# Optimization experiments

Measured on AMD Instinct MI355X. Metric: run time of the kernel, lower is better.

The kernel has to match this reference:

```python
import jax, jax.numpy as jnp
import numpy as np

T, DIM, E, INTER, TOPK = 4096, 1024, 8, 1408, 2


def setup_inputs() -> dict:
    key = jax.random.key(0)
    k_x, k_idx, k1, k2, k3 = jax.random.split(key, 5)
    scale = 1.0 / np.sqrt(DIM)
    return {
        "x": jax.random.normal(k_x, (T, DIM), dtype=jnp.float32),
        "expert_indices": jax.random.randint(k_idx, (T, TOPK), 0, E, dtype=jnp.int64),
        "w1": jax.random.normal(k1, (E, INTER, DIM), dtype=jnp.float32) * scale,
        "w2": jax.random.normal(k2, (E, DIM, INTER), dtype=jnp.float32) * scale,
        "w3": jax.random.normal(k3, (E, INTER, DIM), dtype=jnp.float32) * scale,
    }


def reference(x, expert_indices, w1, w2, w3):
    # All-expert SwiGLU FFN: [T, E, INTER]
    x1 = jax.nn.silu(jnp.einsum('ti,eoi->teo', x, w1))
    x3 = jnp.einsum('ti,eoi->teo', x, w3)
    # Down-projection per expert: [T, E, DIM]
    expert_outs = jnp.einsum('teo,eio->tei', x1 * x3, w2)
    # Gather only the routed experts per token: [T, TOPK, DIM]
    return jnp.take_along_axis(expert_outs, expert_indices[:, :, None], axis=1)
```

## Files before the change

### kernel.cpp

```cpp
#include <hip/hip_runtime.h>

#define TTOK   4096
#define DIMK   1024
#define NEXP   8
#define INTERN 1408
#define NPAIRS 8192

#define BM  128
#define BN  128
#define BK  64
#define NTH 256
#define NTG 512
#define MAXRT (NPAIRS / BM + NEXP - 1)
#define NT1  (INTERN / BN)
#define NT2  (DIMK / BN)

#define CVTBLKS 4096
#define N8X (TTOK * DIMK / 8)
#define N8W (NEXP * INTERN * DIMK / 8)

typedef __attribute__((ext_vector_type(8))) _Float16 half8;
typedef __attribute__((ext_vector_type(2))) _Float16 half2v;
typedef __attribute__((ext_vector_type(4))) float f32x4;

#define MFMAF16(a, b, c) __builtin_amdgcn_mfma_f32_16x16x32_f16((a), (b), (c), 0, 0, 0)

__device__ __forceinline__ void gl_lds16(const void* g, void* l) {
  __builtin_amdgcn_global_load_lds(
      (const __attribute__((address_space(1))) void*)g,
      (__attribute__((address_space(3))) void*)l, 16, 0, 0);
}

__device__ __forceinline__ int xcd_swz(int orig, int G) {
  int q = G >> 3, r = G & 7, x = orig & 7, p = orig >> 3;
  return (x < r ? x * (q + 1) : r * (q + 1) + (x - r) * q) + p;
}

__device__ __forceinline__ void cvt8(const float* __restrict__ src,
                                     unsigned short* __restrict__ dst,
                                     int n8, int tid, int stride) {
  const f32x4* s4 = reinterpret_cast<const f32x4*>(src);
  uint4* d4 = reinterpret_cast<uint4*>(dst);
  for (int i = tid; i < n8; i += stride) {
    f32x4 a = s4[2 * i], b = s4[2 * i + 1];
    uint4 o;
    o.x = __builtin_bit_cast(unsigned int, __builtin_amdgcn_cvt_pkrtz(a[0], a[1]));
    o.y = __builtin_bit_cast(unsigned int, __builtin_amdgcn_cvt_pkrtz(a[2], a[3]));
    o.z = __builtin_bit_cast(unsigned int, __builtin_amdgcn_cvt_pkrtz(b[0], b[1]));
    o.w = __builtin_bit_cast(unsigned int, __builtin_amdgcn_cvt_pkrtz(b[2], b[3]));
    d4[i] = o;
  }
}

__global__ __launch_bounds__(NTH) void prep_kernel(
    const float* __restrict__ x, const float* __restrict__ w1,
    const float* __restrict__ w3, const float* __restrict__ w2,
    unsigned short* __restrict__ xf, unsigned short* __restrict__ w1f,
    unsigned short* __restrict__ w3f, unsigned short* __restrict__ w2f,
    const int* __restrict__ ei, int* __restrict__ offs, int* __restrict__ pairs) {
  const int t = threadIdx.x;

  if (blockIdx.x == CVTBLKS) {
    __shared__ int cnt[NEXP], base[NEXP], cur[NEXP], mode;
    if (t == 0) mode = 0;
    if (t < NEXP) cnt[t] = 0;
    __syncthreads();
    int any = 0;
    for (int i = t; i < NPAIRS / 2; i += NTH) any |= ei[2 * i + 1];
    if (any) atomicOr(&mode, 1);
    __syncthreads();
    const int m32 = mode;
    for (int i = t; i < NPAIRS; i += NTH) {
      int e = (m32 ? ei[i] : ei[2 * i]) & (NEXP - 1);
      atomicAdd(&cnt[e], 1);
    }
    __syncthreads();
    if (t == 0) {
      int s = 0;
      for (int e = 0; e < NEXP; ++e) { base[e] = s; offs[e] = s; s += cnt[e]; }
      offs[NEXP] = s;
    }
    __syncthreads();
    if (t < NEXP) cur[t] = base[t];
    __syncthreads();
    for (int i = t; i < NPAIRS; i += NTH) {
      int e = (m32 ? ei[i] : ei[2 * i]) & (NEXP - 1);
      int p = atomicAdd(&cur[e], 1);
      pairs[p] = i;
    }
    return;
  }

  const int tid = blockIdx.x * NTH + t;
  const int stride = CVTBLKS * NTH;
  cvt8(x,  xf,  N8X, tid, stride);
  cvt8(w1, w1f, N8W, tid, stride);
  cvt8(w3, w3f, N8W, tid, stride);
  cvt8(w2, w2f, N8W, tid, stride);
}

__device__ __forceinline__ bool find_tile(const int* __restrict__ offs, int rt,
                                          int &e, int &row0, int &row_end) {
  int cum = 0;
  for (int i = 0; i < NEXP; ++i) {
    int b = offs[i], en = offs[i + 1];
    int nt = (en - b + BM - 1) / BM;
    if (rt < cum + nt) { e = i; row0 = b + (rt - cum) * BM; row_end = en; return true; }
    cum += nt;
  }
  return false;
}

__global__ __launch_bounds__(NTG, 4) void gemm1_kernel(
    const unsigned short* __restrict__ xf, const unsigned short* __restrict__ w1f,
    const unsigned short* __restrict__ w3f, const int* __restrict__ offs,
    const int* __restrict__ pairs, unsigned short* __restrict__ hf) {
  __shared__ __align__(16) unsigned short At[BM * BK];
  __shared__ __align__(16) unsigned short B1t[BN * BK];
  __shared__ __align__(16) unsigned short B3t[BN * BK];

  const int lid = xcd_swz((int)blockIdx.x, MAXRT * NT1);
  const int rt = lid % MAXRT, nt = lid / MAXRT;
  int e, row0, row_end;
  if (!find_tile(offs, rt, e, row0, row_end)) return;
  const int n0 = nt * BN;
  const int t = threadIdx.x;
  const int ln = t & 63;
  const int wv = t >> 6;
  const int wm = wv >> 2, wn = wv & 3;
  const int fr = ln & 15, fg = ln >> 4;
  const int sr = ln >> 3, sc = ln & 7;
  const int sw = (sc ^ sr) * 8;

  size_t aA[2], aB[2];
#pragma unroll
  for (int c = 0; c < 2; ++c) {
    int row = wv * 16 + c * 8 + sr;
    int p = row0 + row;
    int tok = ((p < row_end) ? pairs[p] : pairs[row0]) >> 1;
    aA[c] = (size_t)tok * DIMK + sw;
    aB[c] = ((size_t)e * INTERN + n0 + row) * DIMK + sw;
  }

  f32x4 acc1[4][2] = {};
  f32x4 acc3[4][2] = {};

  for (int k0 = 0; k0 < DIMK; k0 += BK) {
#pragma unroll
    for (int c = 0; c < 2; ++c)
      gl_lds16(xf + aA[c] + k0, &At[(wv * 16 + c * 8) * BK]);
#pragma unroll
    for (int c = 0; c < 2; ++c)
      gl_lds16(w1f + aB[c] + k0, &B1t[(wv * 16 + c * 8) * BK]);
#pragma unroll
    for (int c = 0; c < 2; ++c)
      gl_lds16(w3f + aB[c] + k0, &B3t[(wv * 16 + c * 8) * BK]);
    __syncthreads();

#pragma unroll
    for (int kk = 0; kk < 2; ++kk) {
      half8 ah[4];
#pragma unroll
      for (int m = 0; m < 4; ++m) {
        int row = wm * 64 + m * 16 + fr;
        ah[m] = *reinterpret_cast<const half8*>(
            &At[row * BK + (((kk * 4 + fg) ^ (fr & 7)) * 8)]);
      }
#pragma unroll
      for (int n = 0; n < 2; ++n) {
        int row = wn * 32 + n * 16 + fr;
        int bo = row * BK + (((kk * 4 + fg) ^ (fr & 7)) * 8);
        half8 b1 = *reinterpret_cast<const half8*>(&B1t[bo]);
        half8 b3 = *reinterpret_cast<const half8*>(&B3t[bo]);
#pragma unroll
        for (int m = 0; m < 4; ++m) {
          acc1[m][n] = MFMAF16(ah[m], b1, acc1[m][n]);
          acc3[m][n] = MFMAF16(ah[m], b3, acc3[m][n]);
        }
      }
    }
    __syncthreads();
  }

#pragma unroll
  for (int m = 0; m < 4; ++m)
#pragma unroll
    for (int n = 0; n < 2; ++n)
#pragma unroll
      for (int r = 0; r < 4; ++r) {
        int p = row0 + wm * 64 + m * 16 + fg * 4 + r;
        if (p < row_end) {
          int col = n0 + wn * 32 + n * 16 + fr;
          float a1 = acc1[m][n][r], a3 = acc3[m][n][r];
          float hv = (a1 / (1.0f + __expf(-a1))) * a3;
          hf[(size_t)p * INTERN + col] =
              __builtin_bit_cast(unsigned short, (_Float16)hv);
        }
      }
}

__global__ __launch_bounds__(NTG, 4) void gemm2_kernel(
    const unsigned short* __restrict__ w2f, const int* __restrict__ offs,
    const int* __restrict__ pairs, const unsigned short* __restrict__ hf,
    float* __restrict__ out) {
  __shared__ __align__(16) unsigned short At[BM * BK];
  __shared__ __align__(16) unsigned short Bt[BN * BK];

  const int lid = xcd_swz((int)blockIdx.x, MAXRT * NT2);
  const int rt = lid % MAXRT, nt = lid / MAXRT;
  int e, row0, row_end;
  if (!find_tile(offs, rt, e, row0, row_end)) return;
  const int n0 = nt * BN;
  const int t = threadIdx.x;
  const int ln = t & 63;
  const int wv = t >> 6;
  const int wm = wv >> 2, wn = wv & 3;
  const int fr = ln & 15, fg = ln >> 4;
  const int sr = ln >> 3, sc = ln & 7;
  const int sw = (sc ^ sr) * 8;

  size_t aA[2], aB[2];
#pragma unroll
  for (int c = 0; c < 2; ++c) {
    int row = wv * 16 + c * 8 + sr;
    int p = row0 + row;
    int ar = (p < row_end) ? p : row0;
    aA[c] = (size_t)ar * INTERN + sw;
    aB[c] = ((size_t)e * DIMK + n0 + row) * INTERN + sw;
  }

  f32x4 acc[4][2] = {};

  for (int k0 = 0; k0 < INTERN; k0 += BK) {
#pragma unroll
    for (int c = 0; c < 2; ++c)
      gl_lds16(hf + aA[c] + k0, &At[(wv * 16 + c * 8) * BK]);
#pragma unroll
    for (int c = 0; c < 2; ++c)
      gl_lds16(w2f + aB[c] + k0, &Bt[(wv * 16 + c * 8) * BK]);
    __syncthreads();

#pragma unroll
    for (int kk = 0; kk < 2; ++kk) {
      half8 ah[4];
#pragma unroll
      for (int m = 0; m < 4; ++m) {
        int row = wm * 64 + m * 16 + fr;
        ah[m] = *reinterpret_cast<const half8*>(
            &At[row * BK + (((kk * 4 + fg) ^ (fr & 7)) * 8)]);
      }
#pragma unroll
      for (int n = 0; n < 2; ++n) {
        int row = wn * 32 + n * 16 + fr;
        half8 b = *reinterpret_cast<const half8*>(
            &Bt[row * BK + (((kk * 4 + fg) ^ (fr & 7)) * 8)]);
#pragma unroll
        for (int m = 0; m < 4; ++m)
          acc[m][n] = MFMAF16(ah[m], b, acc[m][n]);
      }
    }
    __syncthreads();
  }

#pragma unroll
  for (int m = 0; m < 4; ++m)
#pragma unroll
    for (int n = 0; n < 2; ++n)
#pragma unroll
      for (int r = 0; r < 4; ++r) {
        int p = row0 + wm * 64 + m * 16 + fg * 4 + r;
        if (p < row_end) {
          int orow = pairs[p];
          out[(size_t)orow * DIMK + n0 + wn * 32 + n * 16 + fr] = acc[m][n][r];
        }
      }
}

extern "C" void kernel_launch(void* const* d_in, const int* in_sizes, int n_in,
                              void* d_out, int out_size, void* d_ws, size_t ws_size,
                              hipStream_t stream) {
  const float* x  = (const float*)d_in[0];
  const int*   ei = (const int*)d_in[1];
  const float* w1 = (const float*)d_in[2];
  const float* w2 = (const float*)d_in[3];
  const float* w3 = (const float*)d_in[4];
  float* out = (float*)d_out;

  char* ws = (char*)d_ws;
  int* offs  = (int*)ws;
  int* pairs = (int*)(ws + 256);

  const size_t sz_x = (size_t)TTOK * DIMK;
  const size_t sz_w = (size_t)NEXP * INTERN * DIMK;
  size_t off = 65536;
  unsigned short* x_f  = (unsigned short*)(ws + off); off += sz_x * 2;
  unsigned short* w1_f = (unsigned short*)(ws + off); off += sz_w * 2;
  unsigned short* w3_f = (unsigned short*)(ws + off); off += sz_w * 2;
  unsigned short* w2_f = (unsigned short*)(ws + off); off += sz_w * 2;
  unsigned short* h_f  = (unsigned short*)(ws + off);

  prep_kernel<<<CVTBLKS + 1, NTH, 0, stream>>>(
      x, w1, w3, w2, x_f, w1_f, w3_f, w2_f, ei, offs, pairs);
  gemm1_kernel<<<MAXRT * NT1, NTG, 0, stream>>>(x_f, w1_f, w3_f, offs, pairs, h_f);
  gemm2_kernel<<<MAXRT * NT2, NTG, 0, stream>>>(w2_f, offs, pairs, h_f, out);
}
```

Measured before the change: 301.4 us.

## Fuse fp32-to-fp16 weight conversion into GEMM tile loads instead of prepass

Drops the separate prepass that converted all three expert weight tensors to fp16 in global memory. Each GEMM now reads fp32 weights directly, converts them in registers and writes them swizzled into LDS, while x is still converted in a smaller prepass. This removes a full write and re-read of the fp16 weight copies. In exchange, weight tiles are read redundantly in fp32 by every row tile, and the synchronous register-staged loads replace the async global-to-LDS copies.

```diff
diff --git a/kernel.cpp b/kernel.cpp
--- a/kernel.cpp
+++ b/kernel.cpp
@@ -15,12 +15,10 @@
 #define NT1  (INTERN / BN)
 #define NT2  (DIMK / BN)
 
-#define CVTBLKS 4096
+#define XCVB 512
 #define N8X (TTOK * DIMK / 8)
-#define N8W (NEXP * INTERN * DIMK / 8)
 
 typedef __attribute__((ext_vector_type(8))) _Float16 half8;
-typedef __attribute__((ext_vector_type(2))) _Float16 half2v;
 typedef __attribute__((ext_vector_type(4))) float f32x4;
 
 #define MFMAF16(a, b, c) __builtin_amdgcn_mfma_f32_16x16x32_f16((a), (b), (c), 0, 0, 0)
@@ -36,12 +34,59 @@
   return (x < r ? x * (q + 1) : r * (q + 1) + (x - r) * q) + p;
 }
 
-__device__ __forceinline__ void cvt8(const float* __restrict__ src,
-                                     unsigned short* __restrict__ dst,
-                                     int n8, int tid, int stride) {
-  const f32x4* s4 = reinterpret_cast<const f32x4*>(src);
-  uint4* d4 = reinterpret_cast<uint4*>(dst);
-  for (int i = tid; i < n8; i += stride) {
+__device__ __forceinline__ void stage_cvt8(const float* __restrict__ src,
+                                           unsigned short* __restrict__ dst) {
+  f32x4 a = *reinterpret_cast<const f32x4*>(src);
+  f32x4 b = *reinterpret_cast<const f32x4*>(src + 4);
+  uint4 o;
+  o.x = __builtin_bit_cast(unsigned int, __builtin_amdgcn_cvt_pkrtz(a[0], a[1]));
+  o.y = __builtin_bit_cast(unsigned int, __builtin_amdgcn_cvt_pkrtz(a[2], a[3]));
+  o.z = __builtin_bit_cast(unsigned int, __builtin_amdgcn_cvt_pkrtz(b[0], b[1]));
+  o.w = __builtin_bit_cast(unsigned int, __builtin_amdgcn_cvt_pkrtz(b[2], b[3]));
+  *reinterpret_cast<uint4*>(dst) = o;
+}
+
+__global__ __launch_bounds__(NTH) void prep_kernel(
+    const float* __restrict__ x, unsigned short* __restrict__ xf,
+    const int* __restrict__ ei, int* __restrict__ offs, int* __restrict__ pairs) {
+  const int t = threadIdx.x;
+
+  if (blockIdx.x == XCVB) {
+    __shared__ int cnt[NEXP], base[NEXP], cur[NEXP], mode;
+    if (t == 0) mode = 0;
+    if (t < NEXP) cnt[t] = 0;
+    __syncthreads();
+    int any = 0;
+    for (int i = t; i < NPAIRS / 2; i += NTH) any |= ei[2 * i + 1];
+    if (any) atomicOr(&mode, 1);
+    __syncthreads();
+    const int m32 = mode;
+    for (int i = t; i < NPAIRS; i += NTH) {
+      int e = (m32 ? ei[i] : ei[2 * i]) & (NEXP - 1);
+      atomicAdd(&cnt[e], 1);
+    }
+    __syncthreads();
+    if (t == 0) {
+      int s = 0;
+      for (int e = 0; e < NEXP; ++e) { base[e] = s; offs[e] = s; s += cnt[e]; }
+      offs[NEXP] = s;
+    }
+    __syncthreads();
+    if (t < NEXP) cur[t] = base[t];
+    __syncthreads();
+    for (int i = t; i < NPAIRS; i += NTH) {
+      int e = (m32 ? ei[i] : ei[2 * i]) & (NEXP - 1);
+      int p = atomicAdd(&cur[e], 1);
+      pairs[p] = i;
+    }
+    return;
+  }
+
+  const int tid = blockIdx.x * NTH + t;
+  const int stride = XCVB * NTH;
+  const f32x4* s4 = reinterpret_cast<const f32x4*>(x);
+  uint4* d4 = reinterpret_cast<uint4*>(xf);
+  for (int i = tid; i < N8X; i += stride) {
     f32x4 a = s4[2 * i], b = s4[2 * i + 1];
     uint4 o;
     o.x = __builtin_bit_cast(unsigned int, __builtin_amdgcn_cvt_pkrtz(a[0], a[1]));
@@ -50,53 +95,6 @@
     o.w = __builtin_bit_cast(unsigned int, __builtin_amdgcn_cvt_pkrtz(b[2], b[3]));
     d4[i] = o;
   }
-}
-
-__global__ __launch_bounds__(NTH) void prep_kernel(
-    const float* __restrict__ x, const float* __restrict__ w1,
-    const float* __restrict__ w3, const float* __restrict__ w2,
-    unsigned short* __restrict__ xf, unsigned short* __restrict__ w1f,
-    unsigned short* __restrict__ w3f, unsigned short* __restrict__ w2f,
-    const int* __restrict__ ei, int* __restrict__ offs, int* __restrict__ pairs) {
-  const int t = threadIdx.x;
-
-  if (blockIdx.x == CVTBLKS) {
-    __shared__ int cnt[NEXP], base[NEXP], cur[NEXP], mode;
-    if (t == 0) mode = 0;
-    if (t < NEXP) cnt[t] = 0;
-    __syncthreads();
-    int any = 0;
-    for (int i = t; i < NPAIRS / 2; i += NTH) any |= ei[2 * i + 1];
-    if (any) atomicOr(&mode, 1);
-    __syncthreads();
-    const int m32 = mode;
-    for (int i = t; i < NPAIRS; i += NTH) {
-      int e = (m32 ? ei[i] : ei[2 * i]) & (NEXP - 1);
-      atomicAdd(&cnt[e], 1);
-    }
-    __syncthreads();
-    if (t == 0) {
-      int s = 0;
-      for (int e = 0; e < NEXP; ++e) { base[e] = s; offs[e] = s; s += cnt[e]; }
-      offs[NEXP] = s;
-    }
-    __syncthreads();
-    if (t < NEXP) cur[t] = base[t];
-    __syncthreads();
-    for (int i = t; i < NPAIRS; i += NTH) {
-      int e = (m32 ? ei[i] : ei[2 * i]) & (NEXP - 1);
-      int p = atomicAdd(&cur[e], 1);
-      pairs[p] = i;
-    }
-    return;
-  }
-
-  const int tid = blockIdx.x * NTH + t;
-  const int stride = CVTBLKS * NTH;
-  cvt8(x,  xf,  N8X, tid, stride);
-  cvt8(w1, w1f, N8W, tid, stride);
-  cvt8(w3, w3f, N8W, tid, stride);
-  cvt8(w2, w2f, N8W, tid, stride);
 }
 
 __device__ __forceinline__ bool find_tile(const int* __restrict__ offs, int rt,
@@ -112,8 +110,8 @@
 }
 
 __global__ __launch_bounds__(NTG, 4) void gemm1_kernel(
-    const unsigned short* __restrict__ xf, const unsigned short* __restrict__ w1f,
-    const unsigned short* __restrict__ w3f, const int* __restrict__ offs,
+    const unsigned short* __restrict__ xf, const float* __restrict__ w1,
+    const float* __restrict__ w3, const int* __restrict__ offs,
     const int* __restrict__ pairs, unsigned short* __restrict__ hf) {
   __shared__ __align__(16) unsigned short At[BM * BK];
   __shared__ __align__(16) unsigned short B1t[BN * BK];
@@ -133,13 +131,15 @@
   const int sw = (sc ^ sr) * 8;
 
   size_t aA[2], aB[2];
+  int ldsw[2];
 #pragma unroll
   for (int c = 0; c < 2; ++c) {
     int row = wv * 16 + c * 8 + sr;
     int p = row0 + row;
     int tok = ((p < row_end) ? pairs[p] : pairs[row0]) >> 1;
     aA[c] = (size_t)tok * DIMK + sw;
-    aB[c] = ((size_t)e * INTERN + n0 + row) * DIMK + sw;
+    aB[c] = ((size_t)e * INTERN + n0 + row) * DIMK + sc * 8;
+    ldsw[c] = row * BK + (sc ^ sr) * 8;
   }
 
   f32x4 acc1[4][2] = {};
@@ -150,11 +150,10 @@
     for (int c = 0; c < 2; ++c)
       gl_lds16(xf + aA[c] + k0, &At[(wv * 16 + c * 8) * BK]);
 #pragma unroll
-    for (int c = 0; c < 2; ++c)
-      gl_lds16(w1f + aB[c] + k0, &B1t[(wv * 16 + c * 8) * BK]);
-#pragma unroll
-    for (int c = 0; c < 2; ++c)
-      gl_lds16(w3f + aB[c] + k0, &B3t[(wv * 16 + c * 8) * BK]);
+    for (int c = 0; c < 2; ++c) {
+      stage_cvt8(w1 + aB[c] + k0, &B1t[ldsw[c]]);
+      stage_cvt8(w3 + aB[c] + k0, &B3t[ldsw[c]]);
+    }
     __syncthreads();
 
 #pragma unroll
@@ -200,7 +199,7 @@
 }
 
 __global__ __launch_bounds__(NTG, 4) void gemm2_kernel(
-    const unsigned short* __restrict__ w2f, const int* __restrict__ offs,
+    const float* __restrict__ w2, const int* __restrict__ offs,
     const int* __restrict__ pairs, const unsigned short* __restrict__ hf,
     float* __restrict__ out) {
   __shared__ __align__(16) unsigned short At[BM * BK];
@@ -220,13 +219,15 @@
   const int sw = (sc ^ sr) * 8;
 
   size_t aA[2], aB[2];
+  int ldsw[2];
 #pragma unroll
   for (int c = 0; c < 2; ++c) {
     int row = wv * 16 + c * 8 + sr;
     int p = row0 + row;
     int ar = (p < row_end) ? p : row0;
     aA[c] = (size_t)ar * INTERN + sw;
-    aB[c] = ((size_t)e * DIMK + n0 + row) * INTERN + sw;
+    aB[c] = ((size_t)e * DIMK + n0 + row) * INTERN + sc * 8;
+    ldsw[c] = row * BK + (sc ^ sr) * 8;
   }
 
   f32x4 acc[4][2] = {};
@@ -237,7 +238,7 @@
       gl_lds16(hf + aA[c] + k0, &At[(wv * 16 + c * 8) * BK]);
 #pragma unroll
     for (int c = 0; c < 2; ++c)
-      gl_lds16(w2f + aB[c] + k0, &Bt[(wv * 16 + c * 8) * BK]);
+      stage_cvt8(w2 + aB[c] + k0, &Bt[ldsw[c]]);
     __syncthreads();
 
 #pragma unroll
@@ -291,16 +292,11 @@
   int* pairs = (int*)(ws + 256);
 
   const size_t sz_x = (size_t)TTOK * DIMK;
-  const size_t sz_w = (size_t)NEXP * INTERN * DIMK;
   size_t off = 65536;
-  unsigned short* x_f  = (unsigned short*)(ws + off); off += sz_x * 2;
-  unsigned short* w1_f = (unsigned short*)(ws + off); off += sz_w * 2;
-  unsigned short* w3_f = (unsigned short*)(ws + off); off += sz_w * 2;
-  unsigned short* w2_f = (unsigned short*)(ws + off); off += sz_w * 2;
-  unsigned short* h_f  = (unsigned short*)(ws + off);
-
-  prep_kernel<<<CVTBLKS + 1, NTH, 0, stream>>>(
-      x, w1, w3, w2, x_f, w1_f, w3_f, w2_f, ei, offs, pairs);
-  gemm1_kernel<<<MAXRT * NT1, NTG, 0, stream>>>(x_f, w1_f, w3_f, offs, pairs, h_f);
-  gemm2_kernel<<<MAXRT * NT2, NTG, 0, stream>>>(w2_f, offs, pairs, h_f, out);
-}
+  unsigned short* x_f = (unsigned short*)(ws + off); off += sz_x * 2;
+  unsigned short* h_f = (unsigned short*)(ws + off);
+
+  prep_kernel<<<XCVB + 1, NTH, 0, stream>>>(x, x_f, ei, offs, pairs);
+  gemm1_kernel<<<MAXRT * NT1, NTG, 0, stream>>>(x_f, w1, w3, offs, pairs, h_f);
+  gemm2_kernel<<<MAXRT * NT2, NTG, 0, stream>>>(w2, offs, pairs, h_f, out);
+}
```

New measurement: 335.7 us. +11.4%, slower.
